# Performance work log

Measured on AMD Instinct MI355X. Metric: run time of the kernel, lower is better.

The kernel has to match this reference:

```python
import jax, jax.numpy as jnp
import numpy as np

N, E = 50000, 800000
IN_DIM, HID, OUT_DIM, H = 64, 64, 32, 2
NEG_SLOPE = 0.2
TEMP = 1.0
EPS = 1e-20


def gat_conv(x, edge_index, W, att_src, att_dst, bias):
    """PyG GATConv (concat=True, add_self_loops=True, eval mode so dropout off)."""
    n = x.shape[0]
    C = att_src.shape[1]
    # add self-loops (PyG default)
    loops = jnp.arange(n, dtype=edge_index.dtype)
    src = jnp.concatenate([edge_index[0], loops])
    dst = jnp.concatenate([edge_index[1], loops])
    xl = (x @ W).reshape(n, H, C)                      # [N,H,C]
    a_src = (xl * att_src[None]).sum(-1)               # [N,H]
    a_dst = (xl * att_dst[None]).sum(-1)               # [N,H]
    alpha = jax.nn.leaky_relu(a_src[src] + a_dst[dst], NEG_SLOPE)  # [E',H]
    amax = jax.ops.segment_max(alpha, dst, num_segments=n)
    alpha = jnp.exp(alpha - amax[dst])
    denom = jax.ops.segment_sum(alpha, dst, num_segments=n)
    alpha = alpha / (denom[dst] + 1e-16)
    msg = xl[src] * alpha[..., None]                   # [E',H,C]
    out = jax.ops.segment_sum(msg, dst, num_segments=n)
    return out.reshape(n, H * C) + bias


def setup_inputs() -> dict:
    key = jax.random.key(0)
    ks = jax.random.split(key, 18)
    s = 0.05
    inp = {
        'x': jax.random.normal(ks[0], (N, IN_DIM), jnp.float32),
        'edge_index': jax.random.randint(ks[1], (2, E), 0, N, jnp.int64
                                         if jax.config.jax_enable_x64 else jnp.int32).astype(jnp.int32),
        'W0': jax.random.normal(ks[2], (IN_DIM, H * HID)) * s,
        'att_src0': jax.random.normal(ks[3], (H, HID)) * s,
        'att_dst0': jax.random.normal(ks[4], (H, HID)) * s,
        'bias0': jax.random.normal(ks[5], (H * HID,)) * s,
        'fcw0': jax.random.normal(ks[6], (H * HID, HID)) * s,
        'fcb0': jax.random.normal(ks[7], (HID,)) * s,
        'W1': jax.random.normal(ks[8], (HID, H * HID)) * s,
        'att_src1': jax.random.normal(ks[9], (H, HID)) * s,
        'att_dst1': jax.random.normal(ks[10], (H, HID)) * s,
        'bias1': jax.random.normal(ks[11], (H * HID,)) * s,
        'fcw1': jax.random.normal(ks[12], (H * HID, HID)) * s,
        'fcb1': jax.random.normal(ks[13], (HID,)) * s,
        'out_w': jax.random.normal(ks[14], (HID, OUT_DIM)) * s,
        'out_b': jax.random.normal(ks[15], (OUT_DIM,)) * s,
        'gumbel_u': jax.random.uniform(ks[16], (N, OUT_DIM), jnp.float32),
    }
    return inp


def reference(x, edge_index, W0, att_src0, att_dst0, bias0, fcw0, fcb0,
              W1, att_src1, att_dst1, bias1, fcw1, fcb1, out_w, out_b, gumbel_u):
    h = gat_conv(x, edge_index, W0, att_src0, att_dst0, bias0)
    h = jax.nn.elu(h) @ fcw0 + fcb0
    h = gat_conv(h, edge_index, W1, att_src1, att_dst1, bias1)
    h = jax.nn.elu(h) @ fcw1 + fcb1
    logits = h @ out_w + out_b
    g = -jnp.log(-jnp.log(gumbel_u + EPS) + EPS)
    return jax.nn.softmax((logits + g) / TEMP, axis=-1)
```

## Files before the change

kernel.cpp:

```cpp
#include <hip/hip_runtime.h>
#include <hip/hip_fp16.h>
#include <math.h>

#define HEADS 2
#define FDIM 128
#define INDIM 64
#define ODIM 32
#define NEG_SLOPE 0.2f
#define BSH 7
#define BW  128
#define NBLK 128

typedef _Float16 f16x8 __attribute__((ext_vector_type(8)));
typedef float f32x4 __attribute__((ext_vector_type(4)));
union H8 { uint4 u; f16x8 v; __half2 h2[4]; };
union H4 { uint2 u; __half2 h2[2]; };

__device__ __forceinline__ float elu1(float v) { return v > 0.f ? v : __expf(v) - 1.f; }

#define MFMA16(a, b, c) __builtin_amdgcn_mfma_f32_16x16x32_f16((a), (b), (c), 0, 0, 0)

__global__ __launch_bounds__(256) void k_hist2(const int* __restrict__ ei, int E_,
                                               int* __restrict__ cnt, int nb, int epb) {
    __shared__ int h[512];
    int t = threadIdx.x, blk = blockIdx.x;
    for (int i = t; i < nb; i += 256) h[i] = 0;
    __syncthreads();
    int e0 = blk * epb, e1 = min(E_, e0 + epb);
    for (int e = e0 + t; e < e1; e += 256)
        atomicAdd(&h[ei[E_ + e] >> BSH], 1);
    __syncthreads();
    for (int i = t; i < nb; i += 256) cnt[blk * nb + i] = h[i];
}

__global__ __launch_bounds__(512) void k_scanb(const int* __restrict__ cnt,
                                               int* __restrict__ bstart,
                                               int* __restrict__ base, int nb, int E_) {
    __shared__ int sc[512];
    int t = threadIdx.x;
    int tot = 0;
    if (t < nb)
        for (int k = 0; k < NBLK; ++k) tot += cnt[k * nb + t];
    sc[t] = tot;
    __syncthreads();
    for (int o = 1; o < 512; o <<= 1) {
        int add = (t >= o) ? sc[t - o] : 0;
        __syncthreads();
        sc[t] += add;
        __syncthreads();
    }
    int ex = sc[t] - tot;
    if (t < nb) {
        bstart[t] = ex;
        int run = ex;
        for (int k = 0; k < NBLK; ++k) {
            base[k * nb + t] = run;
            run += cnt[k * nb + t];
        }
    }
    if (t == 0) bstart[nb] = E_;
}

__global__ __launch_bounds__(256) void k_scatter2(const int* __restrict__ ei, int E_,
                                                  const int* __restrict__ base,
                                                  unsigned* __restrict__ ebuf,
                                                  int nb, int epb) {
    __shared__ int pcur[512];
    int t = threadIdx.x, blk = blockIdx.x;
    for (int i = t; i < nb; i += 256) pcur[i] = base[blk * nb + i];
    __syncthreads();
    int e0 = blk * epb, e1 = min(E_, e0 + epb);
    for (int e = e0 + t; e < e1; e += 256) {
        int s = ei[e], d = ei[E_ + e];
        int slot = atomicAdd(&pcur[d >> BSH], 1);
        ebuf[slot] = ((unsigned)(d & (BW - 1)) << 25) | (unsigned)s;
    }
}

__global__ __launch_bounds__(256) void k_bfill(const unsigned* __restrict__ ebuf,
                                               const int* __restrict__ bstart,
                                               int* __restrict__ offs,
                                               int* __restrict__ csr_src, int n) {
    __shared__ int hist[BW], sc[BW], pcur[BW];
    int b = blockIdx.x;
    int t = threadIdx.x;
    int base_ = bstart[b];
    int cnt = bstart[b + 1] - base_;
    int d0 = b << BSH;
    if (t < BW) hist[t] = 0;
    __syncthreads();
    for (int i = t; i < cnt; i += 256)
        atomicAdd(&hist[ebuf[base_ + i] >> 25], 1);
    __syncthreads();
    int v = (t < BW) ? hist[t] : 0;
    if (t < BW) sc[t] = v;
    __syncthreads();
    for (int o = 1; o < BW; o <<= 1) {
        int add = (t < BW && t >= o) ? sc[t - o] : 0;
        __syncthreads();
        if (t < BW) sc[t] += add;
        __syncthreads();
    }
    if (t < BW) {
        int abspos = base_ + sc[t] - v;
        pcur[t] = abspos;
        if (d0 + t < n) offs[d0 + t] = abspos;
    }
    __syncthreads();
    for (int i = t; i < cnt; i += 256) {
        unsigned u = ebuf[base_ + i];
        int slot = atomicAdd(&pcur[u >> 25], 1);
        csr_src[slot] = (int)(u & 0x1FFFFFFu);
    }
}

__global__ __launch_bounds__(128) void k_fuse_w(
    const float* __restrict__ W0,
    const float* __restrict__ fcw0, const float* __restrict__ fcb0, const float* __restrict__ W1,
    const float* __restrict__ fcw1, const float* __restrict__ fcb1,
    const float* __restrict__ out_w, const float* __restrict__ out_b,
    __half* __restrict__ W0T, __half* __restrict__ WfT, float* __restrict__ bf,
    __half* __restrict__ WfoT, float* __restrict__ bfo)
{
    int b = blockIdx.x, c = threadIdx.x;
    if (b < 128) {
        float acc = 0.f;
        for (int j = 0; j < 64; ++j) acc = fmaf(fcw0[b * 64 + j], W1[j * 128 + c], acc);
        WfT[c * 128 + b] = __float2half(acc);
    } else if (b == 128) {
        float acc = 0.f;
        for (int j = 0; j < 64; ++j) acc = fmaf(fcb0[j], W1[j * 128 + c], acc);
        bf[c] = acc;
    } else if (b < 257) {
        int k = b - 129;
        if (c < 32) {
            float acc = 0.f;
            for (int j = 0; j < 64; ++j) acc = fmaf(fcw1[k * 64 + j], out_w[j * 32 + c], acc);
            WfoT[c * 128 + k] = __float2half(acc);
        }
    } else if (b == 257) {
        if (c < 32) {
            float acc = 0.f;
            for (int j = 0; j < 64; ++j) acc = fmaf(fcb1[j], out_w[j * 32 + c], acc);
            bfo[c] = acc + out_b[c];
        }
    } else {
        int k = b - 258;
        W0T[c * 64 + k] = __float2half(W0[k * 128 + c]);
    }
}

__global__ __launch_bounds__(256, 2) void k_mm_att1(
    const float* __restrict__ x, const __half* __restrict__ w0t,
    const float* __restrict__ att_src, const float* __restrict__ att_dst,
    __half* __restrict__ xl, float* __restrict__ a_src, float* __restrict__ a_dst,
    int n, int ntiles, int nwaves)
{
    int lane = threadIdx.x & 63;
    int wid = blockIdx.x * 4 + (threadIdx.x >> 6);
    int m = lane & 15, q = lane >> 4;

    H8 A[8][2];
    #pragma unroll
    for (int nt = 0; nt < 8; ++nt)
        #pragma unroll
        for (int kt = 0; kt < 2; ++kt)
            A[nt][kt].u = *(const uint4*)(w0t + (size_t)(nt * 16 + m) * 64 + kt * 32 + q * 8);

    for (int t = wid; t < ntiles; t += nwaves) {
        int rb = t * 16;
        int row = rb + m; if (row >= n) row = n - 1;
        H8 B[2];
        #pragma unroll
        for (int kt = 0; kt < 2; ++kt) {
            const float4* p = (const float4*)(x + (size_t)row * 64 + kt * 32 + q * 8);
            float4 p0 = p[0], p1 = p[1];
            B[kt].h2[0] = __floats2half2_rn(p0.x, p0.y);
            B[kt].h2[1] = __floats2half2_rn(p0.z, p0.w);
            B[kt].h2[2] = __floats2half2_rn(p1.x, p1.y);
            B[kt].h2[3] = __floats2half2_rn(p1.z, p1.w);
        }
        f32x4 acc[8];
        #pragma unroll
        for (int nt = 0; nt < 8; ++nt) {
            acc[nt] = {0.f, 0.f, 0.f, 0.f};
            acc[nt] = MFMA16(A[nt][0].v, B[0].v, acc[nt]);
            acc[nt] = MFMA16(A[nt][1].v, B[1].v, acc[nt]);
        }
        float ps0 = 0.f, ps1 = 0.f, pd0 = 0.f, pd1 = 0.f;
        bool ok = (rb + m) < n;
        #pragma unroll
        for (int nt = 0; nt < 8; ++nt) {
            float4 asv = *(const float4*)(att_src + nt * 16 + q * 4);
            float4 adv = *(const float4*)(att_dst + nt * 16 + q * 4);
            f32x4 d = acc[nt];
            H4 pk;
            pk.h2[0] = __floats2half2_rn(d[0], d[1]);
            pk.h2[1] = __floats2half2_rn(d[2], d[3]);
            if (ok) *(uint2*)(xl + (size_t)(rb + m) * 128 + nt * 16 + q * 4) = pk.u;
            float cs = d[0] * asv.x + d[1] * asv.y + d[2] * asv.z + d[3] * asv.w;
            float cd = d[0] * adv.x + d[1] * adv.y + d[2] * adv.z + d[3] * adv.w;
            if (nt < 4) { ps0 += cs; pd0 += cd; } else { ps1 += cs; pd1 += cd; }
        }
        ps0 += __shfl_xor(ps0, 16, 64); ps0 += __shfl_xor(ps0, 32, 64);
        ps1 += __shfl_xor(ps1, 16, 64); ps1 += __shfl_xor(ps1, 32, 64);
        pd0 += __shfl_xor(pd0, 16, 64); pd0 += __shfl_xor(pd0, 32, 64);
        pd1 += __shfl_xor(pd1, 16, 64); pd1 += __shfl_xor(pd1, 32, 64);
        if (lane < 16 && ok) {
            *(float2*)(a_src + (size_t)(rb + m) * 2) = make_float2(ps0, ps1);
            *(float2*)(a_dst + (size_t)(rb + m) * 2) = make_float2(pd0, pd1);
        }
    }
}

__global__ __launch_bounds__(256, 2) void k_mm_att2(
    const __half* __restrict__ g, const __half* __restrict__ wft, const float* __restrict__ bf,
    const float* __restrict__ att_src, const float* __restrict__ att_dst,
    __half* __restrict__ xl, float* __restrict__ a_src, float* __restrict__ a_dst,
    int n, int ntiles, int nwaves)
{
    int lane = threadIdx.x & 63;
    int wid = blockIdx.x * 4 + (threadIdx.x >> 6);
    int m = lane & 15, q = lane >> 4;

    H8 A[8][4];
    #pragma unroll
    for (int nt = 0; nt < 8; ++nt)
        #pragma unroll
        for (int kt = 0; kt < 4; ++kt)
            A[nt][kt].u = *(const uint4*)(wft + (size_t)(nt * 16 + m) * 128 + kt * 32 + q * 8);

    for (int t = wid; t < ntiles; t += nwaves) {
        int rb = t * 16;
        int row = rb + m; if (row >= n) row = n - 1;
        H8 B[4];
        #pragma unroll
        for (int kt = 0; kt < 4; ++kt) {
            H8 raw;
            raw.u = *(const uint4*)(g + (size_t)row * 128 + kt * 32 + q * 8);
            #pragma unroll
            for (int r = 0; r < 4; ++r) {
                float2 f = __half22float2(raw.h2[r]);
                B[kt].h2[r] = __floats2half2_rn(elu1(f.x), elu1(f.y));
            }
        }
        f32x4 acc[8];
        #pragma unroll
        for (int nt = 0; nt < 8; ++nt) {
            acc[nt] = {0.f, 0.f, 0.f, 0.f};
            #pragma unroll
            for (int kt = 0; kt < 4; ++kt)
                acc[nt] = MFMA16(A[nt][kt].v, B[kt].v, acc[nt]);
        }
        float ps0 = 0.f, ps1 = 0.f, pd0 = 0.f, pd1 = 0.f;
        bool ok = (rb + m) < n;
        #pragma unroll
        for (int nt = 0; nt < 8; ++nt) {
            float4 bfv = *(const float4*)(bf + nt * 16 + q * 4);
            float4 asv = *(const float4*)(att_src + nt * 16 + q * 4);
            float4 adv = *(const float4*)(att_dst + nt * 16 + q * 4);
            f32x4 d = acc[nt];
            d[0] += bfv.x; d[1] += bfv.y; d[2] += bfv.z; d[3] += bfv.w;
            H4 pk;
            pk.h2[0] = __floats2half2_rn(d[0], d[1]);
            pk.h2[1] = __floats2half2_rn(d[2], d[3]);
            if (ok) *(uint2*)(xl + (size_t)(rb + m) * 128 + nt * 16 + q * 4) = pk.u;
            float cs = d[0] * asv.x + d[1] * asv.y + d[2] * asv.z + d[3] * asv.w;
            float cd = d[0] * adv.x + d[1] * adv.y + d[2] * adv.z + d[3] * adv.w;
            if (nt < 4) { ps0 += cs; pd0 += cd; } else { ps1 += cs; pd1 += cd; }
        }
        ps0 += __shfl_xor(ps0, 16, 64); ps0 += __shfl_xor(ps0, 32, 64);
        ps1 += __shfl_xor(ps1, 16, 64); ps1 += __shfl_xor(ps1, 32, 64);
        pd0 += __shfl_xor(pd0, 16, 64); pd0 += __shfl_xor(pd0, 32, 64);
        pd1 += __shfl_xor(pd1, 16, 64); pd1 += __shfl_xor(pd1, 32, 64);
        if (lane < 16 && ok) {
            *(float2*)(a_src + (size_t)(rb + m) * 2) = make_float2(ps0, ps1);
            *(float2*)(a_dst + (size_t)(rb + m) * 2) = make_float2(pd0, pd1);
        }
    }
}

__global__ __launch_bounds__(256, 4) void k_gather(
    const int* __restrict__ offs, const int* __restrict__ csr_src, int E_,
    const __half* __restrict__ xl, const float* __restrict__ a_src,
    const float* __restrict__ a_dst, const float* __restrict__ bias,
    __half* __restrict__ out, int n, int ngrp)
{
    int t = threadIdx.x;
    int lane = t & 63;
    int eh = lane >> 4;
    int cq = lane & 15;
    int h = cq >> 3;
    const float4* bp = (const float4*)(bias + cq * 8);
    float4 b0 = bp[0], b1 = bp[1];

    for (int grp = blockIdx.x; grp < ngrp; grp += gridDim.x) {
        int d = grp * 4 + (t >> 6);
        if (d >= n) continue;
        float ad = a_dst[d * 2 + h];
        int start = offs[d];
        int end = (d + 1 < n) ? offs[d + 1] : E_;
        __half2 hacc[4];
        #pragma unroll
        for (int r = 0; r < 4; ++r) hacc[r] = __floats2half2_rn(0.f, 0.f);
        float den = 0.f;
        for (int j0 = start; j0 < end; j0 += 8) {
            int ja = j0 + eh, jb = j0 + 4 + eh;
            bool va = ja < end, vb = jb < end;
            int sa = va ? csr_src[ja] : d;
            int sb = vb ? csr_src[jb] : d;
            H8 ra, rb;
            ra.u = *(const uint4*)(xl + (size_t)sa * 128 + cq * 8);
            rb.u = *(const uint4*)(xl + (size_t)sb * 128 + cq * 8);
            float aa = a_src[sa * 2 + h] + ad;
            float ab = a_src[sb * 2 + h] + ad;
            aa = (aa >= 0.f) ? aa : NEG_SLOPE * aa;
            ab = (ab >= 0.f) ? ab : NEG_SLOPE * ab;
            float wa = va ? __expf(aa) : 0.f;
            float wb = vb ? __expf(ab) : 0.f;
            __half2 wa2 = __floats2half2_rn(wa, wa);
            __half2 wb2 = __floats2half2_rn(wb, wb);
            #pragma unroll
            for (int r = 0; r < 4; ++r) {
                hacc[r] = __hfma2(ra.h2[r], wa2, hacc[r]);
                hacc[r] = __hfma2(rb.h2[r], wb2, hacc[r]);
            }
            den += wa + wb;
        }
        float acc[8];
        #pragma unroll
        for (int r = 0; r < 4; ++r) {
            float2 f = __half22float2(hacc[r]);
            acc[2 * r] = f.x; acc[2 * r + 1] = f.y;
        }
        if (eh == 0) {
            float a = a_src[d * 2 + h] + ad;
            a = (a >= 0.f) ? a : NEG_SLOPE * a;
            float w = __expf(a);
            H8 raw;
            raw.u = *(const uint4*)(xl + (size_t)d * 128 + cq * 8);
            #pragma unroll
            for (int r = 0; r < 4; ++r) {
                float2 f = __half22float2(raw.h2[r]);
                acc[2 * r]     = fmaf(w, f.x, acc[2 * r]);
                acc[2 * r + 1] = fmaf(w, f.y, acc[2 * r + 1]);
            }
            den += w;
        }
        #pragma unroll
        for (int i = 0; i < 8; ++i) {
            acc[i] += __shfl_xor(acc[i], 16, 64);
            acc[i] += __shfl_xor(acc[i], 32, 64);
        }
        den += __shfl_xor(den, 16, 64);
        den += __shfl_xor(den, 32, 64);
        if (eh == 0) {
            float inv = 1.f / (den + 1e-16f);
            H8 pk;
            pk.h2[0] = __floats2half2_rn(fmaf(acc[0], inv, b0.x), fmaf(acc[1], inv, b0.y));
            pk.h2[1] = __floats2half2_rn(fmaf(acc[2], inv, b0.z), fmaf(acc[3], inv, b0.w));
            pk.h2[2] = __floats2half2_rn(fmaf(acc[4], inv, b1.x), fmaf(acc[5], inv, b1.y));
            pk.h2[3] = __floats2half2_rn(fmaf(acc[6], inv, b1.z), fmaf(acc[7], inv, b1.w));
            *(uint4*)(out + (size_t)d * 128 + cq * 8) = pk.u;
        }
    }
}

__global__ __launch_bounds__(256, 2) void k_mm_final(
    const __half* __restrict__ g, const __half* __restrict__ wfot, const float* __restrict__ bfo,
    const float* __restrict__ gu, float* __restrict__ out, int n, int ntiles, int nwaves)
{
    int lane = threadIdx.x & 63;
    int wid = blockIdx.x * 4 + (threadIdx.x >> 6);
    int m = lane & 15, q = lane >> 4;

    H8 A[2][4];
    #pragma unroll
    for (int nt = 0; nt < 2; ++nt)
        #pragma unroll
        for (int kt = 0; kt < 4; ++kt)
            A[nt][kt].u = *(const uint4*)(wfot + (size_t)(nt * 16 + m) * 128 + kt * 32 + q * 8);

    for (int t = wid; t < ntiles; t += nwaves) {
        int rb = t * 16;
        int row = rb + m; if (row >= n) row = n - 1;
        H8 B[4];
        #pragma unroll
        for (int kt = 0; kt < 4; ++kt) {
            H8 raw;
            raw.u = *(const uint4*)(g + (size_t)row * 128 + kt * 32 + q * 8);
            #pragma unroll
            for (int r = 0; r < 4; ++r) {
                float2 f = __half22float2(raw.h2[r]);
                B[kt].h2[r] = __floats2half2_rn(elu1(f.x), elu1(f.y));
            }
        }
        f32x4 acc[2];
        #pragma unroll
        for (int nt = 0; nt < 2; ++nt) {
            acc[nt] = {0.f, 0.f, 0.f, 0.f};
            #pragma unroll
            for (int kt = 0; kt < 4; ++kt)
                acc[nt] = MFMA16(A[nt][kt].v, B[kt].v, acc[nt]);
        }
        float z[8];
        #pragma unroll
        for (int nt = 0; nt < 2; ++nt) {
            float4 bv = *(const float4*)(bfo + nt * 16 + q * 4);
            float4 uv = *(const float4*)(gu + (size_t)row * 32 + nt * 16 + q * 4);
            z[nt * 4 + 0] = acc[nt][0] + bv.x - __logf(-__logf(uv.x + 1e-20f) + 1e-20f);
            z[nt * 4 + 1] = acc[nt][1] + bv.y - __logf(-__logf(uv.y + 1e-20f) + 1e-20f);
            z[nt * 4 + 2] = acc[nt][2] + bv.z - __logf(-__logf(uv.z + 1e-20f) + 1e-20f);
            z[nt * 4 + 3] = acc[nt][3] + bv.w - __logf(-__logf(uv.w + 1e-20f) + 1e-20f);
        }
        float mx = z[0];
        #pragma unroll
        for (int i = 1; i < 8; ++i) mx = fmaxf(mx, z[i]);
        mx = fmaxf(mx, __shfl_xor(mx, 16, 64));
        mx = fmaxf(mx, __shfl_xor(mx, 32, 64));
        float sum = 0.f;
        #pragma unroll
        for (int i = 0; i < 8; ++i) { z[i] = __expf(z[i] - mx); sum += z[i]; }
        sum += __shfl_xor(sum, 16, 64);
        sum += __shfl_xor(sum, 32, 64);
        float inv = 1.f / sum;
        if (rb + m < n) {
            #pragma unroll
            for (int nt = 0; nt < 2; ++nt) {
                float4 o = make_float4(z[nt * 4 + 0] * inv, z[nt * 4 + 1] * inv,
                                       z[nt * 4 + 2] * inv, z[nt * 4 + 3] * inv);
                *(float4*)(out + (size_t)(rb + m) * 32 + nt * 16 + q * 4) = o;
            }
        }
    }
}

extern "C" void kernel_launch(void* const* d_in, const int* in_sizes, int n_in,
                              void* d_out, int out_size, void* d_ws, size_t ws_size,
                              hipStream_t stream) {
    const float* x        = (const float*)d_in[0];
    const int*   ei       = (const int*)  d_in[1];
    const float* W0       = (const float*)d_in[2];
    const float* att_src0 = (const float*)d_in[3];
    const float* att_dst0 = (const float*)d_in[4];
    const float* bias0    = (const float*)d_in[5];
    const float* fcw0     = (const float*)d_in[6];
    const float* fcb0     = (const float*)d_in[7];
    const float* W1       = (const float*)d_in[8];
    const float* att_src1 = (const float*)d_in[9];
    const float* att_dst1 = (const float*)d_in[10];
    const float* bias1    = (const float*)d_in[11];
    const float* fcw1     = (const float*)d_in[12];
    const float* fcb1     = (const float*)d_in[13];
    const float* out_w    = (const float*)d_in[14];
    const float* out_b    = (const float*)d_in[15];
    const float* gu       = (const float*)d_in[16];

    const int N_ = in_sizes[0] / INDIM;
    const int E_ = in_sizes[1] / 2;
    const int NB = (N_ + BW - 1) / BW;

    float* ws = (float*)d_ws;
    size_t off = 0;
    __half* xl  = (__half*)(ws + off); off += (size_t)N_ * 64;
    __half* gat = (__half*)(ws + off); off += (size_t)N_ * 64;
    float* a_src = ws + off; off += (size_t)N_ * HEADS;
    float* a_dst = ws + off; off += (size_t)N_ * HEADS;
    __half* W0T  = (__half*)(ws + off); off += 128 * 64 / 2;
    __half* WfT  = (__half*)(ws + off); off += 128 * 128 / 2;
    __half* WfoT = (__half*)(ws + off); off += 32 * 128 / 2;
    float* bf    = ws + off; off += 128;
    float* bfo   = ws + off; off += 32;
    int* cnt     = (int*)(ws + off); off += (size_t)NB * NBLK;
    int* base    = (int*)(ws + off); off += (size_t)NB * NBLK;
    int* bstart  = (int*)(ws + off); off += NB + 1;
    int* offs    = (int*)(ws + off); off += N_;
    int* csr_src = (int*)(ws + off); off += E_;
    unsigned* ebuf = (unsigned*)(ws + off); off += E_;

    const int B = 256;
    dim3 blk(B);
    int ngrp   = (N_ + 3) / 4;
    int g_gath = 2048;
    int ntiles = (N_ + 15) / 16;
    int GMM    = 384;
    int nwaves = GMM * 4;
    int epb    = (E_ + NBLK - 1) / NBLK;

    k_hist2    <<<NBLK, blk, 0, stream>>>(ei, E_, cnt, NB, epb);
    k_scanb    <<<1, dim3(512), 0, stream>>>(cnt, bstart, base, NB, E_);
    k_scatter2 <<<NBLK, blk, 0, stream>>>(ei, E_, base, ebuf, NB, epb);
    k_bfill    <<<NB, blk, 0, stream>>>(ebuf, bstart, offs, csr_src, N_);
    k_fuse_w   <<<322, dim3(128), 0, stream>>>(W0, fcw0, fcb0, W1, fcw1, fcb1, out_w, out_b,
                                               W0T, WfT, bf, WfoT, bfo);

    k_mm_att1 <<<GMM,    blk, 0, stream>>>(x, W0T, att_src0, att_dst0, xl, a_src, a_dst,
                                           N_, ntiles, nwaves);
    k_gather  <<<g_gath, blk, 0, stream>>>(offs, csr_src, E_, xl, a_src, a_dst, bias0, gat, N_, ngrp);

    k_mm_att2 <<<GMM,    blk, 0, stream>>>(gat, WfT, bf, att_src1, att_dst1, xl, a_src, a_dst,
                                           N_, ntiles, nwaves);
    k_gather  <<<g_gath, blk, 0, stream>>>(offs, csr_src, E_, xl, a_src, a_dst, bias1, gat, N_, ngrp);

    k_mm_final <<<GMM,   blk, 0, stream>>>(gat, WfoT, bfo, gu, (float*)d_out, N_, ntiles, nwaves);
}
```

Measured before the change: 251.3 us.

## Store projected features as FP8 and gather with fp32 accumulation, 16 edges per step

The projected node features xl are now written as FP8 (4 bytes per 4 values) instead of fp16, halving the bytes gathered per edge in the memory-bound aggregation kernel. The gather loop now processes 16 edges per iteration with four independent loads in flight, and accumulates in fp32 instead of packed fp16. offs gains a sentinel entry so the end-of-segment lookup needs no branch. FP8 storage loses precision in the messages, which risks the accuracy tolerance.

```diff
diff --git a/kernel.cpp b/kernel.cpp
--- a/kernel.cpp
+++ b/kernel.cpp
@@ -13,12 +13,18 @@
 
 typedef _Float16 f16x8 __attribute__((ext_vector_type(8)));
 typedef float f32x4 __attribute__((ext_vector_type(4)));
+typedef float f32x2 __attribute__((ext_vector_type(2)));
 union H8 { uint4 u; f16x8 v; __half2 h2[4]; };
-union H4 { uint2 u; __half2 h2[2]; };
 
 __device__ __forceinline__ float elu1(float v) { return v > 0.f ? v : __expf(v) - 1.f; }
 
 #define MFMA16(a, b, c) __builtin_amdgcn_mfma_f32_16x16x32_f16((a), (b), (c), 0, 0, 0)
+
+__device__ __forceinline__ unsigned pack_fp8x4(float a, float b, float c, float d) {
+    int p = __builtin_amdgcn_cvt_pk_fp8_f32(a, b, 0, false);
+    p = __builtin_amdgcn_cvt_pk_fp8_f32(c, d, p, true);
+    return (unsigned)p;
+}
 
 __global__ __launch_bounds__(256) void k_hist2(const int* __restrict__ ei, int E_,
                                                int* __restrict__ cnt, int nb, int epb) {
@@ -80,10 +86,11 @@
 __global__ __launch_bounds__(256) void k_bfill(const unsigned* __restrict__ ebuf,
                                                const int* __restrict__ bstart,
                                                int* __restrict__ offs,
-                                               int* __restrict__ csr_src, int n) {
+                                               int* __restrict__ csr_src, int n, int E_) {
     __shared__ int hist[BW], sc[BW], pcur[BW];
     int b = blockIdx.x;
     int t = threadIdx.x;
+    if (b == 0 && t == 0) offs[n] = E_;
     int base_ = bstart[b];
     int cnt = bstart[b + 1] - base_;
     int d0 = b << BSH;
@@ -153,7 +160,7 @@
 __global__ __launch_bounds__(256, 2) void k_mm_att1(
     const float* __restrict__ x, const __half* __restrict__ w0t,
     const float* __restrict__ att_src, const float* __restrict__ att_dst,
-    __half* __restrict__ xl, float* __restrict__ a_src, float* __restrict__ a_dst,
+    unsigned char* __restrict__ xl, float* __restrict__ a_src, float* __restrict__ a_dst,
     int n, int ntiles, int nwaves)
 {
     int lane = threadIdx.x & 63;
@@ -194,10 +201,8 @@
             float4 asv = *(const float4*)(att_src + nt * 16 + q * 4);
             float4 adv = *(const float4*)(att_dst + nt * 16 + q * 4);
             f32x4 d = acc[nt];
-            H4 pk;
-            pk.h2[0] = __floats2half2_rn(d[0], d[1]);
-            pk.h2[1] = __floats2half2_rn(d[2], d[3]);
-            if (ok) *(uint2*)(xl + (size_t)(rb + m) * 128 + nt * 16 + q * 4) = pk.u;
+            unsigned pk = pack_fp8x4(d[0], d[1], d[2], d[3]);
+            if (ok) *(unsigned*)(xl + (size_t)(rb + m) * 128 + nt * 16 + q * 4) = pk;
             float cs = d[0] * asv.x + d[1] * asv.y + d[2] * asv.z + d[3] * asv.w;
             float cd = d[0] * adv.x + d[1] * adv.y + d[2] * adv.z + d[3] * adv.w;
             if (nt < 4) { ps0 += cs; pd0 += cd; } else { ps1 += cs; pd1 += cd; }
@@ -216,7 +221,7 @@
 __global__ __launch_bounds__(256, 2) void k_mm_att2(
     const __half* __restrict__ g, const __half* __restrict__ wft, const float* __restrict__ bf,
     const float* __restrict__ att_src, const float* __restrict__ att_dst,
-    __half* __restrict__ xl, float* __restrict__ a_src, float* __restrict__ a_dst,
+    unsigned char* __restrict__ xl, float* __restrict__ a_src, float* __restrict__ a_dst,
     int n, int ntiles, int nwaves)
 {
     int lane = threadIdx.x & 63;
@@ -261,10 +266,8 @@
             float4 adv = *(const float4*)(att_dst + nt * 16 + q * 4);
             f32x4 d = acc[nt];
             d[0] += bfv.x; d[1] += bfv.y; d[2] += bfv.z; d[3] += bfv.w;
-            H4 pk;
-            pk.h2[0] = __floats2half2_rn(d[0], d[1]);
-            pk.h2[1] = __floats2half2_rn(d[2], d[3]);
-            if (ok) *(uint2*)(xl + (size_t)(rb + m) * 128 + nt * 16 + q * 4) = pk.u;
+            unsigned pk = pack_fp8x4(d[0], d[1], d[2], d[3]);
+            if (ok) *(unsigned*)(xl + (size_t)(rb + m) * 128 + nt * 16 + q * 4) = pk;
             float cs = d[0] * asv.x + d[1] * asv.y + d[2] * asv.z + d[3] * asv.w;
             float cd = d[0] * adv.x + d[1] * adv.y + d[2] * adv.z + d[3] * adv.w;
             if (nt < 4) { ps0 += cs; pd0 += cd; } else { ps1 += cs; pd1 += cd; }
@@ -282,7 +285,7 @@
 
 __global__ __launch_bounds__(256, 4) void k_gather(
     const int* __restrict__ offs, const int* __restrict__ csr_src, int E_,
-    const __half* __restrict__ xl, const float* __restrict__ a_src,
+    const unsigned char* __restrict__ xl, const float* __restrict__ a_src,
     const float* __restrict__ a_dst, const float* __restrict__ bias,
     __half* __restrict__ out, int n, int ngrp)
 {
@@ -299,54 +302,54 @@
         if (d >= n) continue;
         float ad = a_dst[d * 2 + h];
         int start = offs[d];
-        int end = (d + 1 < n) ? offs[d + 1] : E_;
-        __half2 hacc[4];
-        #pragma unroll
-        for (int r = 0; r < 4; ++r) hacc[r] = __floats2half2_rn(0.f, 0.f);
+        int end = offs[d + 1];
+        float acc[8] = {0.f, 0.f, 0.f, 0.f, 0.f, 0.f, 0.f, 0.f};
         float den = 0.f;
-        for (int j0 = start; j0 < end; j0 += 8) {
-            int ja = j0 + eh, jb = j0 + 4 + eh;
-            bool va = ja < end, vb = jb < end;
-            int sa = va ? csr_src[ja] : d;
-            int sb = vb ? csr_src[jb] : d;
-            H8 ra, rb;
-            ra.u = *(const uint4*)(xl + (size_t)sa * 128 + cq * 8);
-            rb.u = *(const uint4*)(xl + (size_t)sb * 128 + cq * 8);
-            float aa = a_src[sa * 2 + h] + ad;
-            float ab = a_src[sb * 2 + h] + ad;
-            aa = (aa >= 0.f) ? aa : NEG_SLOPE * aa;
-            ab = (ab >= 0.f) ? ab : NEG_SLOPE * ab;
-            float wa = va ? __expf(aa) : 0.f;
-            float wb = vb ? __expf(ab) : 0.f;
-            __half2 wa2 = __floats2half2_rn(wa, wa);
-            __half2 wb2 = __floats2half2_rn(wb, wb);
-            #pragma unroll
-            for (int r = 0; r < 4; ++r) {
-                hacc[r] = __hfma2(ra.h2[r], wa2, hacc[r]);
-                hacc[r] = __hfma2(rb.h2[r], wb2, hacc[r]);
-            }
-            den += wa + wb;
-        }
-        float acc[8];
-        #pragma unroll
-        for (int r = 0; r < 4; ++r) {
-            float2 f = __half22float2(hacc[r]);
-            acc[2 * r] = f.x; acc[2 * r + 1] = f.y;
+        for (int j0 = start; j0 < end; j0 += 16) {
+            int s0_, s1_, s2_, s3_;
+            int ja = j0 + eh, jb = j0 + 4 + eh, jc = j0 + 8 + eh, jd = j0 + 12 + eh;
+            bool va = ja < end, vb = jb < end, vc = jc < end, vd = jd < end;
+            s0_ = va ? csr_src[ja] : d;
+            s1_ = vb ? csr_src[jb] : d;
+            s2_ = vc ? csr_src[jc] : d;
+            s3_ = vd ? csr_src[jd] : d;
+            uint2 u0 = *(const uint2*)(xl + (size_t)s0_ * 128 + cq * 8);
+            uint2 u1 = *(const uint2*)(xl + (size_t)s1_ * 128 + cq * 8);
+            uint2 u2 = *(const uint2*)(xl + (size_t)s2_ * 128 + cq * 8);
+            uint2 u3 = *(const uint2*)(xl + (size_t)s3_ * 128 + cq * 8);
+            float w0 = a_src[s0_ * 2 + h] + ad;
+            float w1 = a_src[s1_ * 2 + h] + ad;
+            float w2 = a_src[s2_ * 2 + h] + ad;
+            float w3 = a_src[s3_ * 2 + h] + ad;
+            w0 = (w0 >= 0.f) ? w0 : NEG_SLOPE * w0;
+            w1 = (w1 >= 0.f) ? w1 : NEG_SLOPE * w1;
+            w2 = (w2 >= 0.f) ? w2 : NEG_SLOPE * w2;
+            w3 = (w3 >= 0.f) ? w3 : NEG_SLOPE * w3;
+            w0 = va ? __expf(w0) : 0.f;
+            w1 = vb ? __expf(w1) : 0.f;
+            w2 = vc ? __expf(w2) : 0.f;
+            w3 = vd ? __expf(w3) : 0.f;
+            #define ACC8(u, w) { \
+                f32x2 c0 = __builtin_amdgcn_cvt_pk_f32_fp8((u).x, 0); \
+                f32x2 c1 = __builtin_amdgcn_cvt_pk_f32_fp8((u).x, 1); \
+                f32x2 c2 = __builtin_amdgcn_cvt_pk_f32_fp8((u).y, 0); \
+                f32x2 c3 = __builtin_amdgcn_cvt_pk_f32_fp8((u).y, 1); \
+                acc[0] = fmaf((w), c0.x, acc[0]); acc[1] = fmaf((w), c0.y, acc[1]); \
+                acc[2] = fmaf((w), c1.x, acc[2]); acc[3] = fmaf((w), c1.y, acc[3]); \
+                acc[4] = fmaf((w), c2.x, acc[4]); acc[5] = fmaf((w), c2.y, acc[5]); \
+                acc[6] = fmaf((w), c3.x, acc[6]); acc[7] = fmaf((w), c3.y, acc[7]); }
+            ACC8(u0, w0); ACC8(u1, w1); ACC8(u2, w2); ACC8(u3, w3);
+            den += (w0 + w1) + (w2 + w3);
         }
         if (eh == 0) {
             float a = a_src[d * 2 + h] + ad;
             a = (a >= 0.f) ? a : NEG_SLOPE * a;
             float w = __expf(a);
-            H8 raw;
-            raw.u = *(const uint4*)(xl + (size_t)d * 128 + cq * 8);
-            #pragma unroll
-            for (int r = 0; r < 4; ++r) {
-                float2 f = __half22float2(raw.h2[r]);
-                acc[2 * r]     = fmaf(w, f.x, acc[2 * r]);
-                acc[2 * r + 1] = fmaf(w, f.y, acc[2 * r + 1]);
-            }
+            uint2 u = *(const uint2*)(xl + (size_t)d * 128 + cq * 8);
+            ACC8(u, w);
             den += w;
         }
+        #undef ACC8
         #pragma unroll
         for (int i = 0; i < 8; ++i) {
             acc[i] += __shfl_xor(acc[i], 16, 64);
@@ -462,7 +465,7 @@
 
     float* ws = (float*)d_ws;
     size_t off = 0;
-    __half* xl  = (__half*)(ws + off); off += (size_t)N_ * 64;
+    unsigned char* xl = (unsigned char*)(ws + off); off += (size_t)N_ * 32;
     __half* gat = (__half*)(ws + off); off += (size_t)N_ * 64;
     float* a_src = ws + off; off += (size_t)N_ * HEADS;
     float* a_dst = ws + off; off += (size_t)N_ * HEADS;
@@ -474,7 +477,7 @@
     int* cnt     = (int*)(ws + off); off += (size_t)NB * NBLK;
     int* base    = (int*)(ws + off); off += (size_t)NB * NBLK;
     int* bstart  = (int*)(ws + off); off += NB + 1;
-    int* offs    = (int*)(ws + off); off += N_;
+    int* offs    = (int*)(ws + off); off += N_ + 1;
     int* csr_src = (int*)(ws + off); off += E_;
     unsigned* ebuf = (unsigned*)(ws + off); off += E_;
 
@@ -490,7 +493,7 @@
     k_hist2    <<<NBLK, blk, 0, stream>>>(ei, E_, cnt, NB, epb);
     k_scanb    <<<1, dim3(512), 0, stream>>>(cnt, bstart, base, NB, E_);
     k_scatter2 <<<NBLK, blk, 0, stream>>>(ei, E_, base, ebuf, NB, epb);
-    k_bfill    <<<NB, blk, 0, stream>>>(ebuf, bstart, offs, csr_src, N_);
+    k_bfill    <<<NB, blk, 0, stream>>>(ebuf, bstart, offs, csr_src, N_, E_);
     k_fuse_w   <<<322, dim3(128), 0, stream>>>(W0, fcw0, fcb0, W1, fcw1, fcb1, out_w, out_b,
                                                W0T, WfT, bf, WfoT, bfo);
 
```

Measured after the change: 262.2 us. 4.4% more time.

## Fuse histogram, weight folding and first projection into one front kernel

Applied to the files above, without the earlier changes.

Merges the edge-destination histogram, the weight-folding precompute and the first-layer projection/attention kernel into a single launch, with block ranges dispatching to each role. The projection blocks now stage W0 through shared memory and convert it to fp16 fragments themselves, so the separate W0 transpose buffer goes away. This removes two kernel launches and lets independent work run concurrently across blocks. In exchange every block reserves 32KB of shared memory, and the projection role does redundant per-block W0 loads and conversions.

```diff
diff --git a/kernel.cpp b/kernel.cpp
--- a/kernel.cpp
+++ b/kernel.cpp
@@ -5,11 +5,11 @@
 #define HEADS 2
 #define FDIM 128
 #define INDIM 64
-#define ODIM 32
 #define NEG_SLOPE 0.2f
 #define BSH 7
 #define BW  128
 #define NBLK 128
+#define GMM 384
 
 typedef _Float16 f16x8 __attribute__((ext_vector_type(8)));
 typedef float f32x4 __attribute__((ext_vector_type(4)));
@@ -20,17 +20,120 @@
 
 #define MFMA16(a, b, c) __builtin_amdgcn_mfma_f32_16x16x32_f16((a), (b), (c), 0, 0, 0)
 
-__global__ __launch_bounds__(256) void k_hist2(const int* __restrict__ ei, int E_,
-                                               int* __restrict__ cnt, int nb, int epb) {
-    __shared__ int h[512];
-    int t = threadIdx.x, blk = blockIdx.x;
-    for (int i = t; i < nb; i += 256) h[i] = 0;
-    __syncthreads();
-    int e0 = blk * epb, e1 = min(E_, e0 + epb);
-    for (int e = e0 + t; e < e1; e += 256)
-        atomicAdd(&h[ei[E_ + e] >> BSH], 1);
-    __syncthreads();
-    for (int i = t; i < nb; i += 256) cnt[blk * nb + i] = h[i];
+__global__ __launch_bounds__(256, 4) void k_front(
+    const int* __restrict__ ei, int E_, int* __restrict__ cnt, int nb, int epb,
+    const float* __restrict__ fcw0, const float* __restrict__ fcb0, const float* __restrict__ W1,
+    const float* __restrict__ fcw1, const float* __restrict__ fcb1,
+    const float* __restrict__ out_w, const float* __restrict__ out_b,
+    __half* __restrict__ WfT, float* __restrict__ bf,
+    __half* __restrict__ WfoT, float* __restrict__ bfo,
+    const float* __restrict__ x, const float* __restrict__ W0,
+    const float* __restrict__ att_src0, const float* __restrict__ att_dst0,
+    __half* __restrict__ xl, float* __restrict__ a_src, float* __restrict__ a_dst,
+    int n, int ntiles)
+{
+    __shared__ float shw[INDIM * FDIM];
+    int blk = blockIdx.x, t = threadIdx.x;
+
+    if (blk < NBLK) {
+        int* h = (int*)shw;
+        for (int i = t; i < nb; i += 256) h[i] = 0;
+        __syncthreads();
+        int e0 = blk * epb, e1 = min(E_, e0 + epb);
+        for (int e = e0 + t; e < e1; e += 256)
+            atomicAdd(&h[ei[E_ + e] >> BSH], 1);
+        __syncthreads();
+        for (int i = t; i < nb; i += 256) cnt[blk * nb + i] = h[i];
+        return;
+    }
+    if (blk < NBLK + 258) {
+        int b = blk - NBLK, c = t;
+        if (c >= 128) return;
+        if (b < 128) {
+            float acc = 0.f;
+            for (int j = 0; j < 64; ++j) acc = fmaf(fcw0[b * 64 + j], W1[j * 128 + c], acc);
+            WfT[c * 128 + b] = __float2half(acc);
+        } else if (b == 128) {
+            float acc = 0.f;
+            for (int j = 0; j < 64; ++j) acc = fmaf(fcb0[j], W1[j * 128 + c], acc);
+            bf[c] = acc;
+        } else if (b < 257) {
+            int k = b - 129;
+            if (c < 32) {
+                float acc = 0.f;
+                for (int j = 0; j < 64; ++j) acc = fmaf(fcw1[k * 64 + j], out_w[j * 32 + c], acc);
+                WfoT[c * 128 + k] = __float2half(acc);
+            }
+        } else {
+            if (c < 32) {
+                float acc = 0.f;
+                for (int j = 0; j < 64; ++j) acc = fmaf(fcb1[j], out_w[j * 32 + c], acc);
+                bfo[c] = acc + out_b[c];
+            }
+        }
+        return;
+    }
+
+    int lane = t & 63, m = lane & 15, q = lane >> 4;
+    for (int i = t; i < INDIM * FDIM; i += 256) shw[i] = W0[i];
+    __syncthreads();
+    H8 A[8][2];
+    #pragma unroll
+    for (int nt = 0; nt < 8; ++nt)
+        #pragma unroll
+        for (int kt = 0; kt < 2; ++kt)
+            #pragma unroll
+            for (int j = 0; j < 4; ++j) {
+                int k0 = kt * 32 + q * 8 + 2 * j;
+                int c = nt * 16 + m;
+                A[nt][kt].h2[j] = __floats2half2_rn(shw[k0 * 128 + c], shw[(k0 + 1) * 128 + c]);
+            }
+    int wid = (blk - NBLK - 258) * 4 + (t >> 6);
+    int nwaves = GMM * 4;
+    for (int tt = wid; tt < ntiles; tt += nwaves) {
+        int rb = tt * 16;
+        int row = rb + m; if (row >= n) row = n - 1;
+        H8 B[2];
+        #pragma unroll
+        for (int kt = 0; kt < 2; ++kt) {
+            const float4* p = (const float4*)(x + (size_t)row * 64 + kt * 32 + q * 8);
+            float4 p0 = p[0], p1 = p[1];
+            B[kt].h2[0] = __floats2half2_rn(p0.x, p0.y);
+            B[kt].h2[1] = __floats2half2_rn(p0.z, p0.w);
+            B[kt].h2[2] = __floats2half2_rn(p1.x, p1.y);
+            B[kt].h2[3] = __floats2half2_rn(p1.z, p1.w);
+        }
+        f32x4 acc[8];
+        #pragma unroll
+        for (int nt = 0; nt < 8; ++nt) {
+            acc[nt] = {0.f, 0.f, 0.f, 0.f};
+            acc[nt] = MFMA16(A[nt][0].v, B[0].v, acc[nt]);
+            acc[nt] = MFMA16(A[nt][1].v, B[1].v, acc[nt]);
+        }
+        float ps0 = 0.f, ps1 = 0.f, pd0 = 0.f, pd1 = 0.f;
+        bool ok = (rb + m) < n;
+        #pragma unroll
+        for (int nt = 0; nt < 8; ++nt) {
+            float4 asv = *(const float4*)(att_src0 + nt * 16 + q * 4);
+            float4 adv = *(const float4*)(att_dst0 + nt * 16 + q * 4);
+            f32x4 d = acc[nt];
+            H4 pk;
+            pk.h2[0] = __floats2half2_rn(d[0], d[1]);
+            pk.h2[1] = __floats2half2_rn(d[2], d[3]);
+            if (ok) *(uint2*)(xl + (size_t)(rb + m) * 128 + nt * 16 + q * 4) = pk.u;
+            float cs = d[0] * asv.x + d[1] * asv.y + d[2] * asv.z + d[3] * asv.w;
+            float cd = d[0] * adv.x + d[1] * adv.y + d[2] * adv.z + d[3] * adv.w;
+            if (nt < 4) { ps0 += cs; pd0 += cd; } else { ps1 += cs; pd1 += cd; }
+        }
+        ps0 += __shfl_xor(ps0, 16, 64); ps0 += __shfl_xor(ps0, 32, 64);
+        ps1 += __shfl_xor(ps1, 16, 64); ps1 += __shfl_xor(ps1, 32, 64);
+        pd0 += __shfl_xor(pd0, 16, 64); pd0 += __shfl_xor(pd0, 32, 64);
+        pd1 += __shfl_xor(pd1, 16, 64); pd1 += __shfl_xor(pd1, 32, 64);
+        if (lane < 16 && ok) {
+            *(float2*)(a_src + (size_t)(rb + m) * 2) = make_float2(ps0, ps1);
+            *(float2*)(a_dst + (size_t)(rb + m) * 2) = make_float2(pd0, pd1);
+        }
+    }
 }
 
 __global__ __launch_bounds__(512) void k_scanb(const int* __restrict__ cnt,
@@ -111,105 +214,6 @@
         unsigned u = ebuf[base_ + i];
         int slot = atomicAdd(&pcur[u >> 25], 1);
         csr_src[slot] = (int)(u & 0x1FFFFFFu);
-    }
-}
-
-__global__ __launch_bounds__(128) void k_fuse_w(
-    const float* __restrict__ W0,
-    const float* __restrict__ fcw0, const float* __restrict__ fcb0, const float* __restrict__ W1,
-    const float* __restrict__ fcw1, const float* __restrict__ fcb1,
-    const float* __restrict__ out_w, const float* __restrict__ out_b,
-    __half* __restrict__ W0T, __half* __restrict__ WfT, float* __restrict__ bf,
-    __half* __restrict__ WfoT, float* __restrict__ bfo)
-{
-    int b = blockIdx.x, c = threadIdx.x;
-    if (b < 128) {
-        float acc = 0.f;
-        for (int j = 0; j < 64; ++j) acc = fmaf(fcw0[b * 64 + j], W1[j * 128 + c], acc);
-        WfT[c * 128 + b] = __float2half(acc);
-    } else if (b == 128) {
-        float acc = 0.f;
-        for (int j = 0; j < 64; ++j) acc = fmaf(fcb0[j], W1[j * 128 + c], acc);
-        bf[c] = acc;
-    } else if (b < 257) {
-        int k = b - 129;
-        if (c < 32) {
-            float acc = 0.f;
-            for (int j = 0; j < 64; ++j) acc = fmaf(fcw1[k * 64 + j], out_w[j * 32 + c], acc);
-            WfoT[c * 128 + k] = __float2half(acc);
-        }
-    } else if (b == 257) {
-        if (c < 32) {
-            float acc = 0.f;
-            for (int j = 0; j < 64; ++j) acc = fmaf(fcb1[j], out_w[j * 32 + c], acc);
-            bfo[c] = acc + out_b[c];
-        }
-    } else {
-        int k = b - 258;
-        W0T[c * 64 + k] = __float2half(W0[k * 128 + c]);
-    }
-}
-
-__global__ __launch_bounds__(256, 2) void k_mm_att1(
-    const float* __restrict__ x, const __half* __restrict__ w0t,
-    const float* __restrict__ att_src, const float* __restrict__ att_dst,
-    __half* __restrict__ xl, float* __restrict__ a_src, float* __restrict__ a_dst,
-    int n, int ntiles, int nwaves)
-{
-    int lane = threadIdx.x & 63;
-    int wid = blockIdx.x * 4 + (threadIdx.x >> 6);
-    int m = lane & 15, q = lane >> 4;
-
-    H8 A[8][2];
-    #pragma unroll
-    for (int nt = 0; nt < 8; ++nt)
-        #pragma unroll
-        for (int kt = 0; kt < 2; ++kt)
-            A[nt][kt].u = *(const uint4*)(w0t + (size_t)(nt * 16 + m) * 64 + kt * 32 + q * 8);
-
-    for (int t = wid; t < ntiles; t += nwaves) {
-        int rb = t * 16;
-        int row = rb + m; if (row >= n) row = n - 1;
-        H8 B[2];
-        #pragma unroll
-        for (int kt = 0; kt < 2; ++kt) {
-            const float4* p = (const float4*)(x + (size_t)row * 64 + kt * 32 + q * 8);
-            float4 p0 = p[0], p1 = p[1];
-            B[kt].h2[0] = __floats2half2_rn(p0.x, p0.y);
-            B[kt].h2[1] = __floats2half2_rn(p0.z, p0.w);
-            B[kt].h2[2] = __floats2half2_rn(p1.x, p1.y);
-            B[kt].h2[3] = __floats2half2_rn(p1.z, p1.w);
-        }
-        f32x4 acc[8];
-        #pragma unroll
-        for (int nt = 0; nt < 8; ++nt) {
-            acc[nt] = {0.f, 0.f, 0.f, 0.f};
-            acc[nt] = MFMA16(A[nt][0].v, B[0].v, acc[nt]);
-            acc[nt] = MFMA16(A[nt][1].v, B[1].v, acc[nt]);
-        }
-        float ps0 = 0.f, ps1 = 0.f, pd0 = 0.f, pd1 = 0.f;
-        bool ok = (rb + m) < n;
-        #pragma unroll
-        for (int nt = 0; nt < 8; ++nt) {
-            float4 asv = *(const float4*)(att_src + nt * 16 + q * 4);
-            float4 adv = *(const float4*)(att_dst + nt * 16 + q * 4);
-            f32x4 d = acc[nt];
-            H4 pk;
-            pk.h2[0] = __floats2half2_rn(d[0], d[1]);
-            pk.h2[1] = __floats2half2_rn(d[2], d[3]);
-            if (ok) *(uint2*)(xl + (size_t)(rb + m) * 128 + nt * 16 + q * 4) = pk.u;
-            float cs = d[0] * asv.x + d[1] * asv.y + d[2] * asv.z + d[3] * asv.w;
-            float cd = d[0] * adv.x + d[1] * adv.y + d[2] * adv.z + d[3] * adv.w;
-            if (nt < 4) { ps0 += cs; pd0 += cd; } else { ps1 += cs; pd1 += cd; }
-        }
-        ps0 += __shfl_xor(ps0, 16, 64); ps0 += __shfl_xor(ps0, 32, 64);
-        ps1 += __shfl_xor(ps1, 16, 64); ps1 += __shfl_xor(ps1, 32, 64);
-        pd0 += __shfl_xor(pd0, 16, 64); pd0 += __shfl_xor(pd0, 32, 64);
-        pd1 += __shfl_xor(pd1, 16, 64); pd1 += __shfl_xor(pd1, 32, 64);
-        if (lane < 16 && ok) {
-            *(float2*)(a_src + (size_t)(rb + m) * 2) = make_float2(ps0, ps1);
-            *(float2*)(a_dst + (size_t)(rb + m) * 2) = make_float2(pd0, pd1);
-        }
     }
 }
 
@@ -466,7 +470,6 @@
     __half* gat = (__half*)(ws + off); off += (size_t)N_ * 64;
     float* a_src = ws + off; off += (size_t)N_ * HEADS;
     float* a_dst = ws + off; off += (size_t)N_ * HEADS;
-    __half* W0T  = (__half*)(ws + off); off += 128 * 64 / 2;
     __half* WfT  = (__half*)(ws + off); off += 128 * 128 / 2;
     __half* WfoT = (__half*)(ws + off); off += 32 * 128 / 2;
     float* bf    = ws + off; off += 128;
@@ -483,24 +486,19 @@
     int ngrp   = (N_ + 3) / 4;
     int g_gath = 2048;
     int ntiles = (N_ + 15) / 16;
-    int GMM    = 384;
     int nwaves = GMM * 4;
     int epb    = (E_ + NBLK - 1) / NBLK;
 
-    k_hist2    <<<NBLK, blk, 0, stream>>>(ei, E_, cnt, NB, epb);
+    k_front    <<<NBLK + 258 + GMM, blk, 0, stream>>>(
+        ei, E_, cnt, NB, epb,
+        fcw0, fcb0, W1, fcw1, fcb1, out_w, out_b, WfT, bf, WfoT, bfo,
+        x, W0, att_src0, att_dst0, xl, a_src, a_dst, N_, ntiles);
     k_scanb    <<<1, dim3(512), 0, stream>>>(cnt, bstart, base, NB, E_);
     k_scatter2 <<<NBLK, blk, 0, stream>>>(ei, E_, base, ebuf, NB, epb);
     k_bfill    <<<NB, blk, 0, stream>>>(ebuf, bstart, offs, csr_src, N_);
-    k_fuse_w   <<<322, dim3(128), 0, stream>>>(W0, fcw0, fcb0, W1, fcw1, fcb1, out_w, out_b,
-                                               W0T, WfT, bf, WfoT, bfo);
-
-    k_mm_att1 <<<GMM,    blk, 0, stream>>>(x, W0T, att_src0, att_dst0, xl, a_src, a_dst,
-                                           N_, ntiles, nwaves);
-    k_gather  <<<g_gath, blk, 0, stream>>>(offs, csr_src, E_, xl, a_src, a_dst, bias0, gat, N_, ngrp);
-
-    k_mm_att2 <<<GMM,    blk, 0, stream>>>(gat, WfT, bf, att_src1, att_dst1, xl, a_src, a_dst,
-                                           N_, ntiles, nwaves);
-    k_gather  <<<g_gath, blk, 0, stream>>>(offs, csr_src, E_, xl, a_src, a_dst, bias1, gat, N_, ngrp);
-
-    k_mm_final <<<GMM,   blk, 0, stream>>>(gat, WfoT, bfo, gu, (float*)d_out, N_, ntiles, nwaves);
-}
+    k_gather   <<<g_gath, blk, 0, stream>>>(offs, csr_src, E_, xl, a_src, a_dst, bias0, gat, N_, ngrp);
+    k_mm_att2  <<<GMM, blk, 0, stream>>>(gat, WfT, bf, att_src1, att_dst1, xl, a_src, a_dst,
+                                         N_, ntiles, nwaves);
+    k_gather   <<<g_gath, blk, 0, stream>>>(offs, csr_src, E_, xl, a_src, a_dst, bias1, gat, N_, ngrp);
+    k_mm_final <<<GMM, blk, 0, stream>>>(gat, WfoT, bfo, gu, (float*)d_out, N_, ntiles, nwaves);
+}
```

Measured after the change: 257.7 us. 2.6% more time.
